# Kernel tuning notes

Measured on AMD Instinct MI355X. Metric: run time of the kernel, lower is better.

Reference implementation:

```python
import jax, jax.numpy as jnp
import numpy as np

NUM_USERS = 200000
NUM_ITEMS = 100000
EMB = 64
NUM_LAYERS = 3


def setup_inputs() -> dict:
    rng = np.random.default_rng(0)
    E_INTER = 2_000_000
    # unique (user, item) interactions -> faithful to adj[e0, e1] = 1.0 set-semantics
    lin = np.unique(rng.integers(0, NUM_USERS * NUM_ITEMS, size=E_INTER, dtype=np.int64))
    u = (lin // NUM_ITEMS).astype(np.int32)
    it = (lin % NUM_ITEMS).astype(np.int32) + NUM_USERS  # item node ids offset by NUM_USERS
    row = np.concatenate([u, it])  # symmetric bipartite graph, no self-loops
    col = np.concatenate([it, u])
    edge_index = jnp.asarray(np.stack([row, col]), dtype=jnp.int32)  # [2, E]

    key = jax.random.key(0)
    k1, k2 = jax.random.split(key)
    # xavier_uniform on nn.Embedding.weight
    bu = float(np.sqrt(6.0 / (NUM_USERS + EMB)))
    bi = float(np.sqrt(6.0 / (NUM_ITEMS + EMB)))
    user_emb = jax.random.uniform(k1, (NUM_USERS, EMB), jnp.float32, -bu, bu)
    item_emb = jax.random.uniform(k2, (NUM_ITEMS, EMB), jnp.float32, -bi, bi)
    return {"edge_index": edge_index, "user_emb": user_emb, "item_emb": item_emb}


def reference(edge_index, user_emb, item_emb):
    num_users = user_emb.shape[0]
    N = num_users + item_emb.shape[0]
    x = jnp.concatenate([user_emb, item_emb], axis=0)  # ego embeddings [N, D]
    row, col = edge_index[0], edge_index[1]

    # adj has unique off-diagonal edges + eye(N): row-sum degree = edge count + 1
    deg = jax.ops.segment_sum(jnp.ones(row.shape, x.dtype), row, num_segments=N) + 1.0
    dinv = jax.lax.rsqrt(deg)                 # deg >= 1, never inf
    w = (dinv[row] * dinv[col])[:, None]      # per-edge D^-1/2 A D^-1/2 weight
    self_w = (dinv * dinv)[:, None]           # self-loop weight d_i^-1

    acc = x  # sum over layer outputs, including layer 0
    for _ in range(NUM_LAYERS):
        x = jax.ops.segment_sum(w * x[col], row, num_segments=N) + self_w * x
        # dropout is identity in eval mode
        acc = acc + x

    return acc[:num_users], acc[num_users:]
```

## Files before the change

### kernel.cpp

```cpp
#include <hip/hip_runtime.h>
#include <hip/hip_bf16.h>

#define EMB 64
#define BKT_BITS 10
#define BKT_SZ   (1 << BKT_BITS)
#define U_BITS   18
#define U_MASK   ((1u << U_BITS) - 1u)

__device__ __forceinline__ float bf2f(unsigned short h) {
    return __uint_as_float(((unsigned)h) << 16);
}
__device__ __forceinline__ unsigned short f2bf(float f) {
    unsigned u = __float_as_uint(f);
    unsigned r = (u + 0x7fffu + ((u >> 16) & 1u)) >> 16;
    return (unsigned short)r;
}

__global__ void k1_kernel(const int* __restrict__ row, const int* __restrict__ colh,
                          int* __restrict__ urp, int* __restrict__ degit,
                          int NU, int Eh, int urp_blocks) {
    if ((int)blockIdx.x < urp_blocks) {
        int r = blockIdx.x * blockDim.x + threadIdx.x;
        if (r > NU) return;
        if (r == NU) { urp[NU] = Eh; return; }
        int lo = 0, hi = Eh;
        while (lo < hi) {
            int mid = (lo + hi) >> 1;
            if (row[mid] < r) lo = mid + 1; else hi = mid;
        }
        urp[r] = lo;
    } else {
        int e = (blockIdx.x - urp_blocks) * blockDim.x + threadIdx.x;
        if (e < Eh) atomicAdd(&degit[colh[e] - NU], 1);
    }
}

__global__ void k3_kernel(const int* __restrict__ degit, int* __restrict__ excl,
                          int* __restrict__ partials,
                          const int* __restrict__ urp, float* __restrict__ dinv,
                          const float* __restrict__ ue, const float* __restrict__ ie,
                          unsigned short* __restrict__ y0,
                          int NU, int NI, int N, long nu_elems, long total,
                          int nb_s1, int nb_dv) {
    int b = blockIdx.x;
    if (b < nb_s1) {
        __shared__ int sh[256];
        int t = threadIdx.x;
        int base = b * 1024 + t * 4;
        int d0 = (base + 0 < NI) ? degit[base + 0] : 0;
        int d1 = (base + 1 < NI) ? degit[base + 1] : 0;
        int d2 = (base + 2 < NI) ? degit[base + 2] : 0;
        int d3 = (base + 3 < NI) ? degit[base + 3] : 0;
        int tsum = d0 + d1 + d2 + d3;
        sh[t] = tsum;
        __syncthreads();
        for (int off = 1; off < 256; off <<= 1) {
            int v = (t >= off) ? sh[t - off] : 0;
            __syncthreads();
            sh[t] += v;
            __syncthreads();
        }
        int excl_t = sh[t] - tsum;
        if (base + 0 < NI) excl[base + 0] = excl_t;
        if (base + 1 < NI) excl[base + 1] = excl_t + d0;
        if (base + 2 < NI) excl[base + 2] = excl_t + d0 + d1;
        if (base + 3 < NI) excl[base + 3] = excl_t + d0 + d1 + d2;
        if (t == 255) partials[b] = sh[t];
    } else if (b < nb_s1 + nb_dv) {
        int i = (b - nb_s1) * blockDim.x + threadIdx.x;
        if (i >= N) return;
        int d = (i < NU) ? (urp[i + 1] - urp[i]) : degit[i - NU];
        dinv[i] = rsqrtf((float)d + 1.0f);
    } else {
        long j4 = ((long)(b - nb_s1 - nb_dv) * blockDim.x + threadIdx.x) * 4;
        if (j4 >= total) return;
        int node = (int)(j4 >> 6);
        int d = (node < NU) ? (urp[node + 1] - urp[node]) : degit[node - NU];
        float sc = rsqrtf((float)d + 1.0f);
        float4 v = (j4 < nu_elems) ? ((const float4*)ue)[j4 >> 2]
                                   : ((const float4*)ie)[(j4 - nu_elems) >> 2];
        ushort4 o;
        o.x = f2bf(sc * v.x); o.y = f2bf(sc * v.y);
        o.z = f2bf(sc * v.z); o.w = f2bf(sc * v.w);
        ((ushort4*)y0)[j4 >> 2] = o;
    }
}

__global__ void scan2_kernel(int* __restrict__ partials, int nb) {
    __shared__ int sh[512];
    int t = threadIdx.x;
    int v = (t < nb) ? partials[t] : 0;
    sh[t] = v;
    __syncthreads();
    for (int off = 1; off < 512; off <<= 1) {
        int u = (t >= off) ? sh[t - off] : 0;
        __syncthreads();
        sh[t] += u;
        __syncthreads();
    }
    if (t < nb) partials[t] = sh[t] - v;
}

__global__ void scan3_kernel(const int* __restrict__ excl, const int* __restrict__ partials,
                             int* __restrict__ irp, int* __restrict__ cursor,
                             int* __restrict__ bcur, int NI, int Eh) {
    int i = blockIdx.x * blockDim.x + threadIdx.x;
    if (i < NI) {
        int v = excl[i] + partials[i >> 10];
        irp[i] = v;
        cursor[i] = v;
        if ((i & (BKT_SZ - 1)) == 0) bcur[i >> BKT_BITS] = v;
    }
    if (i == NI) irp[NI] = Eh;
}

__global__ void passA_kernel(const int* __restrict__ rowh, const int* __restrict__ colh,
                             int* __restrict__ bcur, unsigned* __restrict__ staging,
                             int Eh, int NU, int NB) {
    __shared__ int cnt[512];
    __shared__ int base[512];
    int t = threadIdx.x;
    for (int j = t; j < NB; j += 256) cnt[j] = 0;
    __syncthreads();
    long cb = (long)blockIdx.x * 1024;
    int b[4], rk[4];
    unsigned pk[4];
#pragma unroll
    for (int j = 0; j < 4; ++j) {
        long e = cb + j * 256 + t;
        if (e < Eh) {
            int u = rowh[e];
            int loc = colh[e] - NU;
            b[j] = loc >> BKT_BITS;
            pk[j] = ((unsigned)(loc & (BKT_SZ - 1)) << U_BITS) | (unsigned)u;
            rk[j] = atomicAdd(&cnt[b[j]], 1);
        } else {
            b[j] = -1;
        }
    }
    __syncthreads();
    for (int j = t; j < NB; j += 256)
        base[j] = cnt[j] ? atomicAdd(&bcur[j], cnt[j]) : 0;
    __syncthreads();
#pragma unroll
    for (int j = 0; j < 4; ++j)
        if (b[j] >= 0) staging[base[b[j]] + rk[j]] = pk[j];
}

__device__ __forceinline__ void spmm_node(
    int i, int q,
    const int* __restrict__ urp, const int* __restrict__ irp,
    const int* __restrict__ colg, const int* __restrict__ icols,
    const float* __restrict__ dinv,
    const unsigned short* __restrict__ yc,
    unsigned short* __restrict__ yn,
    const unsigned short* __restrict__ y0b,
    const unsigned short* __restrict__ y1b,
    float* __restrict__ out, int NU) {
    const int* list;
    int s, e;
    if (i < NU) { s = urp[i]; e = urp[i + 1]; list = colg; }
    else        { int j = i - NU; s = irp[j]; e = irp[j + 1]; list = icols; }
    float di = dinv[i];
    const ushort4* __restrict__ yc4 = (const ushort4*)yc;

    long p = (long)i * 16 + q;
    ushort4 sv = yc4[p];

    float ax = 0.f, ay = 0.f, az = 0.f, aw = 0.f;
    for (int k0 = s; k0 < e; k0 += 8) {
        int   c[8];
        float w[8];
#pragma unroll
        for (int j = 0; j < 8; ++j) {
            int k = k0 + j;
            bool v = (k < e);
            c[j] = v ? list[k] : 0;
            w[j] = v ? 1.0f : 0.0f;
        }
        ushort4 u[8];
#pragma unroll
        for (int j = 0; j < 8; ++j) u[j] = yc4[(long)c[j] * 16 + q];
#pragma unroll
        for (int j = 0; j < 8; ++j) {
            ax += w[j] * bf2f(u[j].x);
            ay += w[j] * bf2f(u[j].y);
            az += w[j] * bf2f(u[j].z);
            aw += w[j] * bf2f(u[j].w);
        }
    }

    ax += bf2f(sv.x);
    ay += bf2f(sv.y);
    az += bf2f(sv.z);
    aw += bf2f(sv.w);

    if (yn) {
        float t = di * di;
        ushort4 o;
        o.x = f2bf(t * ax); o.y = f2bf(t * ay); o.z = f2bf(t * az); o.w = f2bf(t * aw);
        ((ushort4*)yn)[p] = o;
    } else {
        ushort4 a0 = ((const ushort4*)y0b)[p];
        ushort4 a1 = ((const ushort4*)y1b)[p];
        float inv = 1.0f / di;
        float4 o;
        o.x = (bf2f(a0.x) + bf2f(a1.x) + bf2f(sv.x)) * inv + di * ax;
        o.y = (bf2f(a0.y) + bf2f(a1.y) + bf2f(sv.y)) * inv + di * ay;
        o.z = (bf2f(a0.z) + bf2f(a1.z) + bf2f(sv.z)) * inv + di * az;
        o.w = (bf2f(a0.w) + bf2f(a1.w) + bf2f(sv.w)) * inv + di * aw;
        ((float4*)out)[p] = o;
    }
}

__global__ void spmm_kernel(int base, int cnt,
                            const int* __restrict__ urp, const int* __restrict__ irp,
                            const int* __restrict__ colg, const int* __restrict__ icols,
                            const float* __restrict__ dinv,
                            const unsigned short* __restrict__ yc,
                            unsigned short* __restrict__ yn,
                            const unsigned short* __restrict__ y0b,
                            const unsigned short* __restrict__ y1b,
                            float* __restrict__ out, int NU) {
    long t = (long)blockIdx.x * blockDim.x + threadIdx.x;
    int r = (int)(t >> 4);
    if (r >= cnt) return;
    spmm_node(base + r, (int)(t & 15), urp, irp, colg, icols, dinv,
              yc, yn, y0b, y1b, out, NU);
}

__global__ void m6_kernel(const unsigned* __restrict__ staging,
                          const int* __restrict__ irp, int* __restrict__ cursor,
                          int* __restrict__ icols, int NB, int NI,
                          const int* __restrict__ urp,
                          const int* __restrict__ colg,
                          const float* __restrict__ dinv,
                          const unsigned short* __restrict__ yc,
                          unsigned short* __restrict__ yn, int NU) {
    int b = (int)blockIdx.x;
    if (b < NB) {
        int lo = b << BKT_BITS;
        int hi = lo + BKT_SZ; if (hi > NI) hi = NI;
        int start = irp[lo], end = irp[hi];
        for (int k = start + (int)threadIdx.x; k < end; k += 256) {
            unsigned v = staging[k];
            int u   = (int)(v & U_MASK);
            int loc = lo + (int)(v >> U_BITS);
            int pos = atomicAdd(&cursor[loc], 1);
            icols[pos] = u;
        }
    } else {
        long t = (long)(b - NB) * blockDim.x + threadIdx.x;
        int i = (int)(t >> 4);
        if (i >= NU) return;
        spmm_node(i, (int)(t & 15), urp, irp, colg, nullptr, dinv,
                  yc, yn, nullptr, nullptr, nullptr, NU);
    }
}

extern "C" void kernel_launch(void* const* d_in, const int* in_sizes, int n_in,
                              void* d_out, int out_size, void* d_ws, size_t ws_size,
                              hipStream_t stream) {
    const int*   edge_index = (const int*)d_in[0];
    const float* user_emb   = (const float*)d_in[1];
    const float* item_emb   = (const float*)d_in[2];
    float* out = (float*)d_out;

    const int  E  = in_sizes[0] / 2;
    const int  Eh = E / 2;
    const int  NU = in_sizes[1] / EMB;
    const int  NI = in_sizes[2] / EMB;
    const int  N  = NU + NI;
    const long total = (long)N * EMB;

    const int* row = edge_index;
    const int* col = edge_index + E;
    const int* rowh = row;
    const int* colh = col;

    int*   urp      = (int*)d_ws;
    int*   degit    = urp + (NU + 1);
    int*   excl     = degit + NI;
    int*   partials = excl + NI;
    int*   bcur     = partials + 512;
    int*   irp      = bcur + 512;
    int*   cursor   = irp + (NI + 1);
    int*   icols    = cursor + NI;
    float* dinv     = (float*)(icols + Eh);
    unsigned short* y0 = (unsigned short*)(((uintptr_t)(dinv + N) + 127) & ~(uintptr_t)127);
    unsigned short* y1 = y0 + total;
    unsigned short* y2 = y1 + total;
    unsigned* staging = (unsigned*)(y1 + (long)NU * EMB);

    hipMemsetAsync(degit, 0, (size_t)NI * sizeof(int), stream);

    int urp_blocks  = (NU + 256) / 256;
    int ideg_blocks = (Eh + 255) / 256;
    k1_kernel<<<urp_blocks + ideg_blocks, 256, 0, stream>>>(row, colh, urp, degit,
                                                            NU, Eh, urp_blocks);

    int nb_s1 = (NI + 1023) / 1024;
    int nb_dv = (N + 255) / 256;
    int nb_in = (int)((total / 4 + 255) / 256);
    k3_kernel<<<nb_s1 + nb_dv + nb_in, 256, 0, stream>>>(degit, excl, partials,
                                                         urp, dinv, user_emb, item_emb, y0,
                                                         NU, NI, N, (long)NU * EMB, total,
                                                         nb_s1, nb_dv);

    scan2_kernel<<<1, 512, 0, stream>>>(partials, nb_s1);
    scan3_kernel<<<(NI + 1 + 255) / 256, 256, 0, stream>>>(excl, partials, irp, cursor,
                                                           bcur, NI, Eh);

    int NB = (NI + BKT_SZ - 1) >> BKT_BITS;
    int nb_pa = (Eh + 1023) / 1024;
    passA_kernel<<<nb_pa, 256, 0, stream>>>(rowh, colh, bcur, staging, Eh, NU, NB);

    int nb_us = (int)(((long)NU * 16 + 255) / 256);
    m6_kernel<<<NB + nb_us, 256, 0, stream>>>(staging, irp, cursor, icols, NB, NI,
                                              urp, col, dinv, y0, y1, NU);

    int nb_it = (int)(((long)NI * 16 + 255) / 256);
    spmm_kernel<<<nb_it, 256, 0, stream>>>(NU, NI, urp, irp, col, icols, dinv,
                                           y0, y1, nullptr, nullptr, nullptr, NU);

    int nb_all = (int)(((long)N * 16 + 255) / 256);
    spmm_kernel<<<nb_all, 256, 0, stream>>>(0, N, urp, irp, col, icols, dinv,
                                            y1, y2, nullptr, nullptr, nullptr, NU);

    spmm_kernel<<<nb_all, 256, 0, stream>>>(0, N, urp, irp, col, icols, dinv,
                                            y2, nullptr, y0, y1, out, NU);
}
```

Measured before the change: 624.1 us.

## Fuse SpMM layers via bipartite wavefront schedule into per-side kernels

The bipartite structure lets item nodes compute layers 1 and 2 in one kernel, since both read only user rows of y0 and y1. User nodes then compute layers 2 and 3 and the final output together, and items finish layer 3 and their output. This removes one full-graph SpMM pass and reads each adjacency list fewer times, cutting memory traffic and launches. In exchange, each gather loop loads two embedding tables, which raises register pressure and doubles the gather width per edge.

```diff
diff --git a/kernel.cpp b/kernel.cpp
--- a/kernel.cpp
+++ b/kernel.cpp
@@ -147,23 +147,15 @@
         if (b[j] >= 0) staging[base[b[j]] + rk[j]] = pk[j];
 }
 
-__device__ __forceinline__ void spmm_node(
+__device__ __forceinline__ void spmm_node_l0u(
     int i, int q,
-    const int* __restrict__ urp, const int* __restrict__ irp,
-    const int* __restrict__ colg, const int* __restrict__ icols,
+    const int* __restrict__ urp, const int* __restrict__ colg,
     const float* __restrict__ dinv,
     const unsigned short* __restrict__ yc,
-    unsigned short* __restrict__ yn,
-    const unsigned short* __restrict__ y0b,
-    const unsigned short* __restrict__ y1b,
-    float* __restrict__ out, int NU) {
-    const int* list;
-    int s, e;
-    if (i < NU) { s = urp[i]; e = urp[i + 1]; list = colg; }
-    else        { int j = i - NU; s = irp[j]; e = irp[j + 1]; list = icols; }
+    unsigned short* __restrict__ yn) {
+    int s = urp[i], e = urp[i + 1];
     float di = dinv[i];
     const ushort4* __restrict__ yc4 = (const ushort4*)yc;
-
     long p = (long)i * 16 + q;
     ushort4 sv = yc4[p];
 
@@ -175,7 +167,7 @@
         for (int j = 0; j < 8; ++j) {
             int k = k0 + j;
             bool v = (k < e);
-            c[j] = v ? list[k] : 0;
+            c[j] = v ? colg[k] : 0;
             w[j] = v ? 1.0f : 0.0f;
         }
         ushort4 u[8];
@@ -189,44 +181,11 @@
             aw += w[j] * bf2f(u[j].w);
         }
     }
-
-    ax += bf2f(sv.x);
-    ay += bf2f(sv.y);
-    az += bf2f(sv.z);
-    aw += bf2f(sv.w);
-
-    if (yn) {
-        float t = di * di;
-        ushort4 o;
-        o.x = f2bf(t * ax); o.y = f2bf(t * ay); o.z = f2bf(t * az); o.w = f2bf(t * aw);
-        ((ushort4*)yn)[p] = o;
-    } else {
-        ushort4 a0 = ((const ushort4*)y0b)[p];
-        ushort4 a1 = ((const ushort4*)y1b)[p];
-        float inv = 1.0f / di;
-        float4 o;
-        o.x = (bf2f(a0.x) + bf2f(a1.x) + bf2f(sv.x)) * inv + di * ax;
-        o.y = (bf2f(a0.y) + bf2f(a1.y) + bf2f(sv.y)) * inv + di * ay;
-        o.z = (bf2f(a0.z) + bf2f(a1.z) + bf2f(sv.z)) * inv + di * az;
-        o.w = (bf2f(a0.w) + bf2f(a1.w) + bf2f(sv.w)) * inv + di * aw;
-        ((float4*)out)[p] = o;
-    }
-}
-
-__global__ void spmm_kernel(int base, int cnt,
-                            const int* __restrict__ urp, const int* __restrict__ irp,
-                            const int* __restrict__ colg, const int* __restrict__ icols,
-                            const float* __restrict__ dinv,
-                            const unsigned short* __restrict__ yc,
-                            unsigned short* __restrict__ yn,
-                            const unsigned short* __restrict__ y0b,
-                            const unsigned short* __restrict__ y1b,
-                            float* __restrict__ out, int NU) {
-    long t = (long)blockIdx.x * blockDim.x + threadIdx.x;
-    int r = (int)(t >> 4);
-    if (r >= cnt) return;
-    spmm_node(base + r, (int)(t & 15), urp, irp, colg, icols, dinv,
-              yc, yn, y0b, y1b, out, NU);
+    ax += bf2f(sv.x); ay += bf2f(sv.y); az += bf2f(sv.z); aw += bf2f(sv.w);
+    float t = di * di;
+    ushort4 o;
+    o.x = f2bf(t * ax); o.y = f2bf(t * ay); o.z = f2bf(t * az); o.w = f2bf(t * aw);
+    ((ushort4*)yn)[p] = o;
 }
 
 __global__ void m6_kernel(const unsigned* __restrict__ staging,
@@ -235,8 +194,8 @@
                           const int* __restrict__ urp,
                           const int* __restrict__ colg,
                           const float* __restrict__ dinv,
-                          const unsigned short* __restrict__ yc,
-                          unsigned short* __restrict__ yn, int NU) {
+                          const unsigned short* __restrict__ y0,
+                          unsigned short* __restrict__ y1, int NU) {
     int b = (int)blockIdx.x;
     if (b < NB) {
         int lo = b << BKT_BITS;
@@ -253,9 +212,174 @@
         long t = (long)(b - NB) * blockDim.x + threadIdx.x;
         int i = (int)(t >> 4);
         if (i >= NU) return;
-        spmm_node(i, (int)(t & 15), urp, irp, colg, nullptr, dinv,
-                  yc, yn, nullptr, nullptr, nullptr, NU);
-    }
+        spmm_node_l0u(i, (int)(t & 15), urp, colg, dinv, y0, y1);
+    }
+}
+
+__global__ void d2_kernel(const int* __restrict__ irp, const int* __restrict__ icols,
+                          const float* __restrict__ dinv,
+                          const unsigned short* __restrict__ y0,
+                          unsigned short* __restrict__ y1,
+                          unsigned short* __restrict__ y2, int NU, int NI) {
+    long t = (long)blockIdx.x * blockDim.x + threadIdx.x;
+    int j = (int)(t >> 4);
+    if (j >= NI) return;
+    int q = (int)(t & 15);
+    int i = NU + j;
+    int s = irp[j], e = irp[j + 1];
+    float di = dinv[i];
+    const ushort4* __restrict__ y04 = (const ushort4*)y0;
+    const ushort4* __restrict__ y14 = (const ushort4*)y1;
+    long p = (long)i * 16 + q;
+    ushort4 sv0 = y04[p];
+
+    float a0x = 0.f, a0y = 0.f, a0z = 0.f, a0w = 0.f;
+    float a1x = 0.f, a1y = 0.f, a1z = 0.f, a1w = 0.f;
+    for (int k0 = s; k0 < e; k0 += 8) {
+        long  off[8];
+        float w[8];
+#pragma unroll
+        for (int jj = 0; jj < 8; ++jj) {
+            int k = k0 + jj;
+            bool v = (k < e);
+            int c = v ? icols[k] : 0;
+            off[jj] = (long)c * 16 + q;
+            w[jj] = v ? 1.0f : 0.0f;
+        }
+        ushort4 u0[8], u1[8];
+#pragma unroll
+        for (int jj = 0; jj < 8; ++jj) { u0[jj] = y04[off[jj]]; u1[jj] = y14[off[jj]]; }
+#pragma unroll
+        for (int jj = 0; jj < 8; ++jj) {
+            a0x += w[jj] * bf2f(u0[jj].x); a0y += w[jj] * bf2f(u0[jj].y);
+            a0z += w[jj] * bf2f(u0[jj].z); a0w += w[jj] * bf2f(u0[jj].w);
+            a1x += w[jj] * bf2f(u1[jj].x); a1y += w[jj] * bf2f(u1[jj].y);
+            a1z += w[jj] * bf2f(u1[jj].z); a1w += w[jj] * bf2f(u1[jj].w);
+        }
+    }
+    float sq = di * di;
+    a0x += bf2f(sv0.x); a0y += bf2f(sv0.y); a0z += bf2f(sv0.z); a0w += bf2f(sv0.w);
+    ushort4 o1;
+    o1.x = f2bf(sq * a0x); o1.y = f2bf(sq * a0y);
+    o1.z = f2bf(sq * a0z); o1.w = f2bf(sq * a0w);
+    ((ushort4*)y1)[p] = o1;
+    a1x += bf2f(o1.x); a1y += bf2f(o1.y); a1z += bf2f(o1.z); a1w += bf2f(o1.w);
+    ushort4 o2;
+    o2.x = f2bf(sq * a1x); o2.y = f2bf(sq * a1y);
+    o2.z = f2bf(sq * a1z); o2.w = f2bf(sq * a1w);
+    ((ushort4*)y2)[p] = o2;
+}
+
+__global__ void d3_kernel(const int* __restrict__ urp, const int* __restrict__ colg,
+                          const float* __restrict__ dinv,
+                          const unsigned short* __restrict__ y0,
+                          const unsigned short* __restrict__ y1,
+                          unsigned short* __restrict__ y2,
+                          float* __restrict__ out, int NU) {
+    long t = (long)blockIdx.x * blockDim.x + threadIdx.x;
+    int i = (int)(t >> 4);
+    if (i >= NU) return;
+    int q = (int)(t & 15);
+    int s = urp[i], e = urp[i + 1];
+    float di = dinv[i];
+    const ushort4* __restrict__ y04 = (const ushort4*)y0;
+    const ushort4* __restrict__ y14 = (const ushort4*)y1;
+    const ushort4* __restrict__ y24 = (const ushort4*)y2;
+    long p = (long)i * 16 + q;
+    ushort4 sv0 = y04[p];
+    ushort4 sv1 = y14[p];
+
+    float a1x = 0.f, a1y = 0.f, a1z = 0.f, a1w = 0.f;
+    float a2x = 0.f, a2y = 0.f, a2z = 0.f, a2w = 0.f;
+    for (int k0 = s; k0 < e; k0 += 8) {
+        long  off[8];
+        float w[8];
+#pragma unroll
+        for (int jj = 0; jj < 8; ++jj) {
+            int k = k0 + jj;
+            bool v = (k < e);
+            int c = v ? colg[k] : 0;
+            off[jj] = (long)c * 16 + q;
+            w[jj] = v ? 1.0f : 0.0f;
+        }
+        ushort4 u1[8], u2[8];
+#pragma unroll
+        for (int jj = 0; jj < 8; ++jj) { u1[jj] = y14[off[jj]]; u2[jj] = y24[off[jj]]; }
+#pragma unroll
+        for (int jj = 0; jj < 8; ++jj) {
+            a1x += w[jj] * bf2f(u1[jj].x); a1y += w[jj] * bf2f(u1[jj].y);
+            a1z += w[jj] * bf2f(u1[jj].z); a1w += w[jj] * bf2f(u1[jj].w);
+            a2x += w[jj] * bf2f(u2[jj].x); a2y += w[jj] * bf2f(u2[jj].y);
+            a2z += w[jj] * bf2f(u2[jj].z); a2w += w[jj] * bf2f(u2[jj].w);
+        }
+    }
+    float sq = di * di;
+    a1x += bf2f(sv1.x); a1y += bf2f(sv1.y); a1z += bf2f(sv1.z); a1w += bf2f(sv1.w);
+    ushort4 o2;
+    o2.x = f2bf(sq * a1x); o2.y = f2bf(sq * a1y);
+    o2.z = f2bf(sq * a1z); o2.w = f2bf(sq * a1w);
+    ((ushort4*)y2)[p] = o2;
+    a2x += bf2f(o2.x); a2y += bf2f(o2.y); a2z += bf2f(o2.z); a2w += bf2f(o2.w);
+    float inv = 1.0f / di;
+    float4 o;
+    o.x = (bf2f(sv0.x) + bf2f(sv1.x) + bf2f(o2.x)) * inv + di * a2x;
+    o.y = (bf2f(sv0.y) + bf2f(sv1.y) + bf2f(o2.y)) * inv + di * a2y;
+    o.z = (bf2f(sv0.z) + bf2f(sv1.z) + bf2f(o2.z)) * inv + di * a2z;
+    o.w = (bf2f(sv0.w) + bf2f(sv1.w) + bf2f(o2.w)) * inv + di * a2w;
+    ((float4*)out)[p] = o;
+}
+
+__global__ void d4_kernel(const int* __restrict__ irp, const int* __restrict__ icols,
+                          const float* __restrict__ dinv,
+                          const unsigned short* __restrict__ y0,
+                          const unsigned short* __restrict__ y1,
+                          const unsigned short* __restrict__ y2,
+                          float* __restrict__ out, int NU, int NI) {
+    long t = (long)blockIdx.x * blockDim.x + threadIdx.x;
+    int j = (int)(t >> 4);
+    if (j >= NI) return;
+    int q = (int)(t & 15);
+    int i = NU + j;
+    int s = irp[j], e = irp[j + 1];
+    float di = dinv[i];
+    const ushort4* __restrict__ y04 = (const ushort4*)y0;
+    const ushort4* __restrict__ y14 = (const ushort4*)y1;
+    const ushort4* __restrict__ y24 = (const ushort4*)y2;
+    long p = (long)i * 16 + q;
+    ushort4 sv0 = y04[p];
+    ushort4 sv1 = y14[p];
+    ushort4 sv2 = y24[p];
+
+    float ax = 0.f, ay = 0.f, az = 0.f, aw = 0.f;
+    for (int k0 = s; k0 < e; k0 += 8) {
+        int   c[8];
+        float w[8];
+#pragma unroll
+        for (int jj = 0; jj < 8; ++jj) {
+            int k = k0 + jj;
+            bool v = (k < e);
+            c[jj] = v ? icols[k] : 0;
+            w[jj] = v ? 1.0f : 0.0f;
+        }
+        ushort4 u[8];
+#pragma unroll
+        for (int jj = 0; jj < 8; ++jj) u[jj] = y24[(long)c[jj] * 16 + q];
+#pragma unroll
+        for (int jj = 0; jj < 8; ++jj) {
+            ax += w[jj] * bf2f(u[jj].x);
+            ay += w[jj] * bf2f(u[jj].y);
+            az += w[jj] * bf2f(u[jj].z);
+            aw += w[jj] * bf2f(u[jj].w);
+        }
+    }
+    ax += bf2f(sv2.x); ay += bf2f(sv2.y); az += bf2f(sv2.z); aw += bf2f(sv2.w);
+    float inv = 1.0f / di;
+    float4 o;
+    o.x = (bf2f(sv0.x) + bf2f(sv1.x) + bf2f(sv2.x)) * inv + di * ax;
+    o.y = (bf2f(sv0.y) + bf2f(sv1.y) + bf2f(sv2.y)) * inv + di * ay;
+    o.z = (bf2f(sv0.z) + bf2f(sv1.z) + bf2f(sv2.z)) * inv + di * az;
+    o.w = (bf2f(sv0.w) + bf2f(sv1.w) + bf2f(sv2.w)) * inv + di * aw;
+    ((float4*)out)[p] = o;
 }
 
 extern "C" void kernel_launch(void* const* d_in, const int* in_sizes, int n_in,
@@ -320,13 +444,9 @@
                                               urp, col, dinv, y0, y1, NU);
 
     int nb_it = (int)(((long)NI * 16 + 255) / 256);
-    spmm_kernel<<<nb_it, 256, 0, stream>>>(NU, NI, urp, irp, col, icols, dinv,
-                                           y0, y1, nullptr, nullptr, nullptr, NU);
-
-    int nb_all = (int)(((long)N * 16 + 255) / 256);
-    spmm_kernel<<<nb_all, 256, 0, stream>>>(0, N, urp, irp, col, icols, dinv,
-                                            y1, y2, nullptr, nullptr, nullptr, NU);
-
-    spmm_kernel<<<nb_all, 256, 0, stream>>>(0, N, urp, irp, col, icols, dinv,
-                                            y2, nullptr, y0, y1, out, NU);
-}
+    d2_kernel<<<nb_it, 256, 0, stream>>>(irp, icols, dinv, y0, y1, y2, NU, NI);
+
+    d3_kernel<<<nb_us, 256, 0, stream>>>(urp, col, dinv, y0, y1, y2, out, NU);
+
+    d4_kernel<<<nb_it, 256, 0, stream>>>(irp, icols, dinv, y0, y1, y2, out, NU, NI);
+}
```

Measured after the change: 602.3 us. -3.5%, faster.
